# Optimization experiments

Hardware: AMD Instinct MI355X
Metric: run time of the kernel (lower is better)

## Reference

```python
import jax, jax.numpy as jnp
import numpy as np

NUM_NODES = 100000
OUT_CHANNELS = 64
NUM_EDGES = 3200000


def setup_inputs() -> dict:
    key = jax.random.key(0)
    k1, k2, k3 = jax.random.split(key, 3)
    edge_index = jax.random.randint(k1, (2, NUM_EDGES), 0, NUM_NODES, dtype=jnp.int64) if jax.config.jax_enable_x64 else jax.random.randint(k1, (2, NUM_EDGES), 0, NUM_NODES, dtype=jnp.int32)
    # nn.Linear default init: U(-1/sqrt(fan_in), 1/sqrt(fan_in)); use randn-scale for a correctness baseline
    W_weight = jax.random.normal(k2, (OUT_CHANNELS, NUM_NODES), dtype=jnp.float32) * (1.0 / np.sqrt(NUM_NODES))
    W_bias = jax.random.normal(k3, (OUT_CHANNELS,), dtype=jnp.float32) * (1.0 / np.sqrt(NUM_NODES))
    return {"edge_index": edge_index, "W_weight": W_weight, "W_bias": W_bias}


def reference(edge_index, W_weight, W_bias):
    # A is the [N, N] binary COO adjacency (duplicate edges sum, matching
    # an uncoalesced torch sparse COO matmul). logits = A @ W_weight.T + b.
    num_nodes = W_weight.shape[1]
    row = edge_index[0] - jnp.min(edge_index[0])  # row = row - row.min()
    col = edge_index[1]
    Wt = W_weight.T  # [N, C]
    # SpMM as gather + segment-sum: logits[i] = sum_{(i,j) in E} Wt[j]
    logits = jax.ops.segment_sum(Wt[col], row, num_segments=num_nodes)  # [N, C]
    logits = logits + W_bias
    return jax.nn.log_softmax(logits, axis=1)
```

## Files before the change

### kernel.cpp

```cpp
#include <hip/hip_runtime.h>
#include <hip/hip_bf16.h>
#include <hip/hip_fp8.h>
#include <limits.h>

#define NUM_NODES 100000
#define OUT_CH 64
#define NUM_EDGES 3200000
#define BROWS 64
#define BSHIFT 6
#define NBUCK 1563
#define NBUCK_EXT 3125
#define NPBLK 256
#define EPB (NUM_EDGES / NPBLK)
#define I4PB (EPB / 4)
#define STAGECAP 4096
#define NTRANS 1563
#define FP8_SCALE 256.0f
#define FP8_INV (1.0f / 256.0f)

typedef float v2f __attribute__((ext_vector_type(2)));

__device__ __forceinline__ float fp8_decode_slow(unsigned b) {
    unsigned s = b >> 7, e = (b >> 3) & 0xF, m = b & 7;
    float v = (e == 0) ? ldexpf((float)m, -9) : ldexpf((float)(8 + m), (int)e - 10);
    return s ? -v : v;
}

__global__ __launch_bounds__(256) void LINK_62689342652831_mth_kernel(
    const float* __restrict__ W, unsigned char* __restrict__ Wt8,
    const int* __restrict__ rows, int* __restrict__ minp, int* __restrict__ hist2d) {
    __shared__ float tile[64][65];
    if (blockIdx.x < NTRANS) {
        int n0 = blockIdx.x * 64;
        int tx = threadIdx.x & 63;
        int ty = threadIdx.x >> 6;
        for (int c = ty; c < 64; c += 4) {
            int n = n0 + tx;
            tile[c][tx] = (n < NUM_NODES) ? W[(size_t)c * NUM_NODES + n] : 0.0f;
        }
        __syncthreads();
        for (int i = ty; i < 64; i += 4) {
            int n = n0 + i;
            if (n < NUM_NODES) {
                __hip_fp8_e4m3 q(FP8_SCALE * tile[tx][i]);
                Wt8[(size_t)n * OUT_CH + tx] = *reinterpret_cast<unsigned char*>(&q);
            }
        }
    } else {
        int blk = blockIdx.x - NTRANS;
        int* h = (int*)tile;
        int* sm = (int*)tile + 2048;
        for (int i = threadIdx.x; i < NBUCK; i += 256) h[i] = 0;
        __syncthreads();
        const int4* r4 = (const int4*)rows;
        int m = INT_MAX;
        for (int i = threadIdx.x; i < I4PB; i += 256) {
            int4 v = r4[blk * I4PB + i];
            m = min(m, min(min(v.x, v.y), min(v.z, v.w)));
            atomicAdd(&h[(unsigned)v.x >> BSHIFT], 1);
            atomicAdd(&h[(unsigned)v.y >> BSHIFT], 1);
            atomicAdd(&h[(unsigned)v.z >> BSHIFT], 1);
            atomicAdd(&h[(unsigned)v.w >> BSHIFT], 1);
        }
        for (int off = 32; off > 0; off >>= 1) m = min(m, __shfl_xor(m, off, 64));
        if ((threadIdx.x & 63) == 0) sm[threadIdx.x >> 6] = m;
        __syncthreads();
        for (int i = threadIdx.x; i < NBUCK; i += 256) hist2d[blk * NBUCK + i] = h[i];
        if (threadIdx.x == 0)
            atomicMin(minp, min(min(sm[0], sm[1]), min(sm[2], sm[3])));
    }
}

__global__ __launch_bounds__(512) void LINK_62689342652831_colscan_kernel(
    int* __restrict__ hist2d, int* __restrict__ totals) {
    int lane = threadIdx.x & 63;
    int wid = threadIdx.x >> 6;
    int b = blockIdx.x * 8 + wid;
    if (b >= NBUCK) return;
    int carry = 0;
    for (int rnd = 0; rnd < NPBLK / 64; ++rnd) {
        int blk = rnd * 64 + lane;
        int v = hist2d[blk * NBUCK + b];
        int x = v;
        for (int off = 1; off < 64; off <<= 1) {
            int y = __shfl_up(x, off, 64);
            if (lane >= off) x += y;
        }
        hist2d[blk * NBUCK + b] = x - v + carry;
        carry += __shfl(x, 63, 64);
    }
    if (lane == 0) totals[b] = carry;
}

__global__ __launch_bounds__(1024) void LINK_62689342652831_bscan_kernel(
    const int* __restrict__ totals, int* __restrict__ bstart) {
    __shared__ int ss[1024];
    int t = threadIdx.x;
    int i0 = 2 * t, i1 = 2 * t + 1;
    int v0 = (i0 < NBUCK) ? totals[i0] : 0;
    int v1 = (i1 < NBUCK) ? totals[i1] : 0;
    int p1 = v0 + v1;
    ss[t] = p1;
    __syncthreads();
    for (int off = 1; off < 1024; off <<= 1) {
        int x = (t >= off) ? ss[t - off] : 0;
        __syncthreads();
        ss[t] += x;
        __syncthreads();
    }
    int texcl = ss[t] - p1;
    if (i0 < NBUCK) bstart[i0] = texcl;
    if (i1 < NBUCK) bstart[i1] = texcl + v0;
    if (t == 1023) bstart[NBUCK] = ss[1023];
}

__global__ __launch_bounds__(512) void LINK_62689342652831_part_kernel(
    const int* __restrict__ rows, const int* __restrict__ cols,
    const int* __restrict__ hist2d, const int* __restrict__ bstart,
    unsigned int* __restrict__ packed) {
    __shared__ int offs_l[NBUCK];
    __shared__ int lcur[NBUCK];
    int blk = blockIdx.x;
    for (int i = threadIdx.x; i < NBUCK; i += 512) {
        offs_l[i] = bstart[i] + hist2d[blk * NBUCK + i];
        lcur[i] = 0;
    }
    __syncthreads();
    const int4* r4 = (const int4*)rows;
    const int4* c4 = (const int4*)cols;
    for (int i = threadIdx.x; i < I4PB; i += 512) {
        int4 rv = r4[blk * I4PB + i];
        int4 cv = c4[blk * I4PB + i];
#pragma unroll
        for (int k = 0; k < 4; ++k) {
            int r = (k == 0) ? rv.x : (k == 1) ? rv.y : (k == 2) ? rv.z : rv.w;
            int c = (k == 0) ? cv.x : (k == 1) ? cv.y : (k == 2) ? cv.z : cv.w;
            int b = (unsigned)r >> BSHIFT;
            int pos = offs_l[b] + atomicAdd(&lcur[b], 1);
            packed[pos] = ((unsigned)(r & (BROWS - 1)) << 17) | (unsigned)c;
        }
    }
}

__global__ __launch_bounds__(256) void LINK_62689342652831_spmm_kernel(
    const unsigned int* __restrict__ packed, const int* __restrict__ bstart,
    const unsigned char* __restrict__ Wt8, const float* __restrict__ bias,
    const int* __restrict__ minp, float* __restrict__ out) {
    __shared__ unsigned int sorted[STAGECAP];
    __shared__ int rhist[BROWS];
    __shared__ int rstart[BROWS + 1];
    __shared__ int rcur[BROWS];

    int lane = threadIdx.x & 63;
    int wid = threadIdx.x >> 6;
    int b = blockIdx.x;
    int minv = *minp;
    if (b * BROWS - minv >= NUM_NODES) return;
    int s = 0, e = 0;
    if (b < NBUCK) { s = bstart[b]; e = bstart[b + 1]; }
    int n = e - s;

    if (n <= STAGECAP) {
        if (threadIdx.x < BROWS) rhist[threadIdx.x] = 0;
        __syncthreads();
        for (int i = threadIdx.x; i < n; i += 256)
            atomicAdd(&rhist[packed[s + i] >> 17], 1);
        __syncthreads();
        if (threadIdx.x < 64) {
            int c0 = rhist[lane];
            int x0 = c0;
            for (int off = 1; off < 64; off <<= 1) {
                int y0 = __shfl_up(x0, off, 64);
                if (lane >= off) x0 += y0;
            }
            rstart[lane] = x0 - c0;
            rcur[lane] = x0 - c0;
            if (lane == 63) rstart[64] = x0;
        }
        __syncthreads();
        for (int i = threadIdx.x; i < n; i += 256) {
            unsigned int u = packed[s + i];
            int pos = atomicAdd(&rcur[u >> 17], 1);
            sorted[pos] = u;
        }
        __syncthreads();

        const unsigned int* Wt1 = (const unsigned int*)Wt8;
        int q = lane >> 4;
        int ql = lane & 15;
        float b0 = bias[4 * ql], b1 = bias[4 * ql + 1],
              b2 = bias[4 * ql + 2], b3 = bias[4 * ql + 3];

        for (int r = wid; r < BROWS; r += 4) {
            int gr = b * BROWS + r - minv;
            if (gr < 0 || gr >= NUM_NODES) continue;
            int s0 = rstart[r], e0 = rstart[r + 1];
            float a0 = 0, a1 = 0, a2 = 0, a3 = 0;
            int i = s0 + q;
            for (; i + 4 < e0; i += 8) {
                unsigned int ua = sorted[i], ub = sorted[i + 4];
                unsigned int wa = Wt1[(size_t)(ua & 0x1FFFF) * 16 + ql];
                unsigned int wb = Wt1[(size_t)(ub & 0x1FFFF) * 16 + ql];
#if __has_builtin(__builtin_amdgcn_cvt_pk_f32_fp8)
                v2f la = __builtin_amdgcn_cvt_pk_f32_fp8((int)wa, false);
                v2f ha = __builtin_amdgcn_cvt_pk_f32_fp8((int)wa, true);
                v2f lb = __builtin_amdgcn_cvt_pk_f32_fp8((int)wb, false);
                v2f hb = __builtin_amdgcn_cvt_pk_f32_fp8((int)wb, true);
                a0 += la.x + lb.x; a1 += la.y + lb.y;
                a2 += ha.x + hb.x; a3 += ha.y + hb.y;
#else
                a0 += fp8_decode_slow(wa & 0xFF) + fp8_decode_slow(wb & 0xFF);
                a1 += fp8_decode_slow((wa >> 8) & 0xFF) + fp8_decode_slow((wb >> 8) & 0xFF);
                a2 += fp8_decode_slow((wa >> 16) & 0xFF) + fp8_decode_slow((wb >> 16) & 0xFF);
                a3 += fp8_decode_slow(wa >> 24) + fp8_decode_slow(wb >> 24);
#endif
            }
            for (; i < e0; i += 4) {
                unsigned int w = Wt1[(size_t)(sorted[i] & 0x1FFFF) * 16 + ql];
#if __has_builtin(__builtin_amdgcn_cvt_pk_f32_fp8)
                v2f lo = __builtin_amdgcn_cvt_pk_f32_fp8((int)w, false);
                v2f hi = __builtin_amdgcn_cvt_pk_f32_fp8((int)w, true);
                a0 += lo.x; a1 += lo.y; a2 += hi.x; a3 += hi.y;
#else
                a0 += fp8_decode_slow(w & 0xFF);
                a1 += fp8_decode_slow((w >> 8) & 0xFF);
                a2 += fp8_decode_slow((w >> 16) & 0xFF);
                a3 += fp8_decode_slow(w >> 24);
#endif
            }
            a0 += __shfl_xor(a0, 32, 64); a1 += __shfl_xor(a1, 32, 64);
            a2 += __shfl_xor(a2, 32, 64); a3 += __shfl_xor(a3, 32, 64);
            a0 += __shfl_xor(a0, 16, 64); a1 += __shfl_xor(a1, 16, 64);
            a2 += __shfl_xor(a2, 16, 64); a3 += __shfl_xor(a3, 16, 64);

            float x0 = a0 * FP8_INV + b0, x1 = a1 * FP8_INV + b1;
            float x2 = a2 * FP8_INV + b2, x3 = a3 * FP8_INV + b3;
            float m = fmaxf(fmaxf(x0, x1), fmaxf(x2, x3));
            for (int off = 8; off > 0; off >>= 1) m = fmaxf(m, __shfl_xor(m, off, 64));
            float ssum = expf(x0 - m) + expf(x1 - m) + expf(x2 - m) + expf(x3 - m);
            for (int off = 8; off > 0; off >>= 1) ssum += __shfl_xor(ssum, off, 64);
            float l = m + logf(ssum);
            if (lane < 16) {
                float4 o = {x0 - l, x1 - l, x2 - l, x3 - l};
                *(float4*)&out[(size_t)gr * OUT_CH + 4 * ql] = o;
            }
        }
    } else {
        float* acc = (float*)sorted;
        for (int i = threadIdx.x; i < BROWS * OUT_CH; i += 256) acc[i] = 0.0f;
        __syncthreads();
        for (int i = s + wid; i < e; i += 4) {
            unsigned int u = packed[i];
            float v = fp8_decode_slow(Wt8[(size_t)(u & 0x1FFFF) * OUT_CH + lane]);
            atomicAdd(&acc[(u >> 17) * OUT_CH + lane], v);
        }
        __syncthreads();
        float bsv = bias[lane];
        for (int r = wid; r < BROWS; r += 4) {
            int gr = b * BROWS + r - minv;
            if (gr < 0 || gr >= NUM_NODES) continue;
            float x = acc[r * OUT_CH + lane] * FP8_INV + bsv;
            float m = x;
            for (int off = 32; off > 0; off >>= 1) m = fmaxf(m, __shfl_xor(m, off, 64));
            float ex = expf(x - m);
            float ssum = ex;
            for (int off = 32; off > 0; off >>= 1) ssum += __shfl_xor(ssum, off, 64);
            out[(size_t)gr * OUT_CH + lane] = x - m - logf(ssum);
        }
    }
}

__global__ void LINK_62689342652831_minf_kernel(const int* __restrict__ rows, int n,
                                                int* __restrict__ minp) {
    int tid = blockIdx.x * blockDim.x + threadIdx.x;
    int stride = gridDim.x * blockDim.x;
    int m = INT_MAX;
    for (int i = tid; i < n; i += stride) m = min(m, rows[i]);
    for (int off = 32; off > 0; off >>= 1) m = min(m, __shfl_xor(m, off, 64));
    if ((threadIdx.x & 63) == 0) atomicMin(minp, m);
}

__global__ void LINK_62689342652831_scatter_kernel(const int* __restrict__ rows,
                                                   const int* __restrict__ cols,
                                                   const float* __restrict__ W,
                                                   const int* __restrict__ minp,
                                                   float* __restrict__ out) {
    int lane = threadIdx.x & 63;
    int gw = (blockIdx.x * blockDim.x + threadIdx.x) >> 6;
    int nw = (gridDim.x * blockDim.x) >> 6;
    int minv = *minp;
    for (int e = gw; e < NUM_EDGES; e += nw) {
        int r = rows[e] - minv;
        int c = cols[e];
        float v = W[(size_t)lane * NUM_NODES + c];
        unsafeAtomicAdd(&out[(size_t)r * 64 + lane], v);
    }
}

__global__ void LINK_62689342652831_logsoftmax_kernel(float* __restrict__ out,
                                                      const float* __restrict__ bias) {
    int lane = threadIdx.x & 63;
    int gw = (blockIdx.x * blockDim.x + threadIdx.x) >> 6;
    int nw = (gridDim.x * blockDim.x) >> 6;
    float b = bias[lane];
    for (int r = gw; r < NUM_NODES; r += nw) {
        float x = out[(size_t)r * 64 + lane] + b;
        float m = x;
        for (int off = 32; off > 0; off >>= 1) m = fmaxf(m, __shfl_xor(m, off, 64));
        float e = expf(x - m);
        float s = e;
        for (int off = 32; off > 0; off >>= 1) s += __shfl_xor(s, off, 64);
        out[(size_t)r * 64 + lane] = x - m - logf(s);
    }
}

extern "C" void kernel_launch(void* const* d_in, const int* in_sizes, int n_in,
                              void* d_out, int out_size, void* d_ws, size_t ws_size,
                              hipStream_t stream) {
    const int* edges = (const int*)d_in[0];
    const int* rows = edges;
    const int* cols = edges + NUM_EDGES;
    const float* W = (const float*)d_in[1];
    const float* bias = (const float*)d_in[2];
    float* out = (float*)d_out;

    char* ws = (char*)d_ws;
    const size_t OFF_MIN = 0;
    const size_t OFF_TOT = 1024;
    const size_t OFF_BSTART = 16384;
    const size_t OFF_H2D = 32768;
    const size_t OFF_PACKED = 2 * 1024 * 1024;
    const size_t OFF_WT8 = OFF_PACKED + (size_t)NUM_EDGES * 4;
    const size_t need = OFF_WT8 + (size_t)NUM_NODES * OUT_CH;

    int* minp = (int*)(ws + OFF_MIN);
    int* totals = (int*)(ws + OFF_TOT);
    int* bstart = (int*)(ws + OFF_BSTART);
    int* hist2d = (int*)(ws + OFF_H2D);
    unsigned int* packed = (unsigned int*)(ws + OFF_PACKED);
    unsigned char* Wt8 = (unsigned char*)(ws + OFF_WT8);

    hipMemsetAsync(minp, 0x7f, sizeof(int), stream);

    if (ws_size >= need) {
        LINK_62689342652831_mth_kernel<<<NTRANS + NPBLK, 256, 0, stream>>>(W, Wt8, rows,
                                                                           minp, hist2d);
        LINK_62689342652831_colscan_kernel<<<(NBUCK + 7) / 8, 512, 0, stream>>>(hist2d, totals);
        LINK_62689342652831_bscan_kernel<<<1, 1024, 0, stream>>>(totals, bstart);
        LINK_62689342652831_part_kernel<<<NPBLK, 512, 0, stream>>>(rows, cols, hist2d,
                                                                   bstart, packed);
        LINK_62689342652831_spmm_kernel<<<NBUCK_EXT, 256, 0, stream>>>(packed, bstart, Wt8,
                                                                       bias, minp, out);
    } else {
        LINK_62689342652831_minf_kernel<<<2048, 256, 0, stream>>>(rows, NUM_EDGES, minp);
        hipMemsetAsync(d_out, 0, (size_t)out_size * sizeof(float), stream);
        LINK_62689342652831_scatter_kernel<<<2048, 256, 0, stream>>>(rows, cols, W, minp, out);
        LINK_62689342652831_logsoftmax_kernel<<<4096, 256, 0, stream>>>(out, bias);
    }
}
```

Baseline: 127.4 us.

## Fuse transpose, histogram, scans and partition into one cooperative kernel

Replaces the four preprocessing kernels (transpose/histogram, column scan, bucket scan, partition) with a single cooperative launch that uses grid-wide syncs between phases. Each block keeps its packed (row,col) edge words in shared memory (EPB entries), so the partition phase does not reload the column array from global memory. This removes three kernel launches and their inter-kernel gaps. In exchange it relies on only 256 blocks, which must all be co-resident; this limits parallelism for the transpose and colscan phases and adds grid.sync costs. The large shared-memory footprint (about 50KB) lowers occupancy.

```diff
diff --git a/kernel.cpp b/kernel.cpp
--- a/kernel.cpp
+++ b/kernel.cpp
@@ -1,7 +1,10 @@
 #include <hip/hip_runtime.h>
 #include <hip/hip_bf16.h>
 #include <hip/hip_fp8.h>
+#include <hip/hip_cooperative_groups.h>
 #include <limits.h>
+
+namespace cg = cooperative_groups;
 
 #define NUM_NODES 100000
 #define OUT_CH 64
@@ -26,118 +29,138 @@
     return s ? -v : v;
 }
 
-__global__ __launch_bounds__(256) void LINK_62689342652831_mth_kernel(
+__global__ __launch_bounds__(512) void LINK_62689342652831_coop_kernel(
     const float* __restrict__ W, unsigned char* __restrict__ Wt8,
-    const int* __restrict__ rows, int* __restrict__ minp, int* __restrict__ hist2d) {
-    __shared__ float tile[64][65];
-    if (blockIdx.x < NTRANS) {
-        int n0 = blockIdx.x * 64;
-        int tx = threadIdx.x & 63;
-        int ty = threadIdx.x >> 6;
-        for (int c = ty; c < 64; c += 4) {
-            int n = n0 + tx;
-            tile[c][tx] = (n < NUM_NODES) ? W[(size_t)c * NUM_NODES + n] : 0.0f;
-        }
-        __syncthreads();
-        for (int i = ty; i < 64; i += 4) {
+    const int* __restrict__ rows, const int* __restrict__ cols,
+    int* __restrict__ minp, int* __restrict__ hist2d, int* __restrict__ totals,
+    int* __restrict__ bstart, unsigned int* __restrict__ packed) {
+    cg::grid_group grid = cg::this_grid();
+    __shared__ unsigned int pk[EPB];
+    __shared__ int h[NBUCK];
+    __shared__ int lcur[NBUCK];
+    __shared__ int sm8[8];
+
+    int tid = threadIdx.x;
+    int blk = blockIdx.x;
+    int lane = tid & 63;
+    int wid = tid >> 6;
+
+    float(*tile)[65] = (float(*)[65])pk;
+    for (int tb = blk; tb < NTRANS; tb += NPBLK) {
+        int n0 = tb * 64;
+        for (int c = wid; c < 64; c += 8) {
+            int n = n0 + lane;
+            tile[c][lane] = (n < NUM_NODES) ? W[(size_t)c * NUM_NODES + n] : 0.0f;
+        }
+        __syncthreads();
+        for (int i = wid; i < 64; i += 8) {
             int n = n0 + i;
             if (n < NUM_NODES) {
-                __hip_fp8_e4m3 q(FP8_SCALE * tile[tx][i]);
-                Wt8[(size_t)n * OUT_CH + tx] = *reinterpret_cast<unsigned char*>(&q);
-            }
-        }
-    } else {
-        int blk = blockIdx.x - NTRANS;
-        int* h = (int*)tile;
-        int* sm = (int*)tile + 2048;
-        for (int i = threadIdx.x; i < NBUCK; i += 256) h[i] = 0;
-        __syncthreads();
-        const int4* r4 = (const int4*)rows;
-        int m = INT_MAX;
-        for (int i = threadIdx.x; i < I4PB; i += 256) {
-            int4 v = r4[blk * I4PB + i];
-            m = min(m, min(min(v.x, v.y), min(v.z, v.w)));
-            atomicAdd(&h[(unsigned)v.x >> BSHIFT], 1);
-            atomicAdd(&h[(unsigned)v.y >> BSHIFT], 1);
-            atomicAdd(&h[(unsigned)v.z >> BSHIFT], 1);
-            atomicAdd(&h[(unsigned)v.w >> BSHIFT], 1);
-        }
-        for (int off = 32; off > 0; off >>= 1) m = min(m, __shfl_xor(m, off, 64));
-        if ((threadIdx.x & 63) == 0) sm[threadIdx.x >> 6] = m;
-        __syncthreads();
-        for (int i = threadIdx.x; i < NBUCK; i += 256) hist2d[blk * NBUCK + i] = h[i];
-        if (threadIdx.x == 0)
-            atomicMin(minp, min(min(sm[0], sm[1]), min(sm[2], sm[3])));
-    }
-}
-
-__global__ __launch_bounds__(512) void LINK_62689342652831_colscan_kernel(
-    int* __restrict__ hist2d, int* __restrict__ totals) {
-    int lane = threadIdx.x & 63;
-    int wid = threadIdx.x >> 6;
-    int b = blockIdx.x * 8 + wid;
-    if (b >= NBUCK) return;
-    int carry = 0;
-    for (int rnd = 0; rnd < NPBLK / 64; ++rnd) {
-        int blk = rnd * 64 + lane;
-        int v = hist2d[blk * NBUCK + b];
-        int x = v;
-        for (int off = 1; off < 64; off <<= 1) {
-            int y = __shfl_up(x, off, 64);
-            if (lane >= off) x += y;
-        }
-        hist2d[blk * NBUCK + b] = x - v + carry;
-        carry += __shfl(x, 63, 64);
-    }
-    if (lane == 0) totals[b] = carry;
-}
-
-__global__ __launch_bounds__(1024) void LINK_62689342652831_bscan_kernel(
-    const int* __restrict__ totals, int* __restrict__ bstart) {
-    __shared__ int ss[1024];
-    int t = threadIdx.x;
-    int i0 = 2 * t, i1 = 2 * t + 1;
-    int v0 = (i0 < NBUCK) ? totals[i0] : 0;
-    int v1 = (i1 < NBUCK) ? totals[i1] : 0;
-    int p1 = v0 + v1;
-    ss[t] = p1;
-    __syncthreads();
-    for (int off = 1; off < 1024; off <<= 1) {
-        int x = (t >= off) ? ss[t - off] : 0;
-        __syncthreads();
-        ss[t] += x;
-        __syncthreads();
-    }
-    int texcl = ss[t] - p1;
-    if (i0 < NBUCK) bstart[i0] = texcl;
-    if (i1 < NBUCK) bstart[i1] = texcl + v0;
-    if (t == 1023) bstart[NBUCK] = ss[1023];
-}
-
-__global__ __launch_bounds__(512) void LINK_62689342652831_part_kernel(
-    const int* __restrict__ rows, const int* __restrict__ cols,
-    const int* __restrict__ hist2d, const int* __restrict__ bstart,
-    unsigned int* __restrict__ packed) {
-    __shared__ int offs_l[NBUCK];
-    __shared__ int lcur[NBUCK];
-    int blk = blockIdx.x;
-    for (int i = threadIdx.x; i < NBUCK; i += 512) {
-        offs_l[i] = bstart[i] + hist2d[blk * NBUCK + i];
-        lcur[i] = 0;
-    }
+                __hip_fp8_e4m3 q(FP8_SCALE * tile[lane][i]);
+                Wt8[(size_t)n * OUT_CH + lane] = *reinterpret_cast<unsigned char*>(&q);
+            }
+        }
+        __syncthreads();
+    }
+
+    for (int i = tid; i < NBUCK; i += 512) h[i] = 0;
     __syncthreads();
     const int4* r4 = (const int4*)rows;
     const int4* c4 = (const int4*)cols;
-    for (int i = threadIdx.x; i < I4PB; i += 512) {
+    uint4* pk4 = (uint4*)pk;
+    int m = INT_MAX;
+    for (int i = tid; i < I4PB; i += 512) {
         int4 rv = r4[blk * I4PB + i];
         int4 cv = c4[blk * I4PB + i];
+        m = min(m, min(min(rv.x, rv.y), min(rv.z, rv.w)));
+        atomicAdd(&h[(unsigned)rv.x >> BSHIFT], 1);
+        atomicAdd(&h[(unsigned)rv.y >> BSHIFT], 1);
+        atomicAdd(&h[(unsigned)rv.z >> BSHIFT], 1);
+        atomicAdd(&h[(unsigned)rv.w >> BSHIFT], 1);
+        uint4 p;
+        p.x = ((unsigned)(rv.x & (BROWS - 1)) << 17) | (unsigned)cv.x;
+        p.y = ((unsigned)(rv.y & (BROWS - 1)) << 17) | (unsigned)cv.y;
+        p.z = ((unsigned)(rv.z & (BROWS - 1)) << 17) | (unsigned)cv.z;
+        p.w = ((unsigned)(rv.w & (BROWS - 1)) << 17) | (unsigned)cv.w;
+        pk4[i] = p;
+    }
+    for (int off = 32; off > 0; off >>= 1) m = min(m, __shfl_xor(m, off, 64));
+    if (lane == 0) sm8[wid] = m;
+    __syncthreads();
+    if (tid == 0) {
+        int mm = sm8[0];
+#pragma unroll
+        for (int k = 1; k < 8; ++k) mm = min(mm, sm8[k]);
+        atomicMin(minp, mm);
+    }
+    for (int i = tid; i < NBUCK; i += 512) hist2d[blk * NBUCK + i] = h[i];
+    grid.sync();
+
+    {
+        int b = blk * 8 + wid;
+        if (b < NBUCK) {
+            int carry = 0;
+            for (int rnd = 0; rnd < NPBLK / 64; ++rnd) {
+                int bb = rnd * 64 + lane;
+                int v = hist2d[bb * NBUCK + b];
+                int x = v;
+                for (int off = 1; off < 64; off <<= 1) {
+                    int y = __shfl_up(x, off, 64);
+                    if (lane >= off) x += y;
+                }
+                hist2d[bb * NBUCK + b] = x - v + carry;
+                carry += __shfl(x, 63, 64);
+            }
+            if (lane == 0) totals[b] = carry;
+        }
+    }
+    grid.sync();
+
+    if (blk == 0) {
+        int* ss = lcur;
+        int v0 = 0, v1 = 0, v2 = 0, v3 = 0;
+        int base = tid * 4;
+        if (base + 0 < NBUCK) v0 = totals[base + 0];
+        if (base + 1 < NBUCK) v1 = totals[base + 1];
+        if (base + 2 < NBUCK) v2 = totals[base + 2];
+        if (base + 3 < NBUCK) v3 = totals[base + 3];
+        int run = v0 + v1 + v2 + v3;
+        ss[tid] = run;
+        __syncthreads();
+        for (int off = 1; off < 512; off <<= 1) {
+            int x = (tid >= off) ? ss[tid - off] : 0;
+            __syncthreads();
+            ss[tid] += x;
+            __syncthreads();
+        }
+        int acc = ss[tid] - run;
+        if (base + 0 < NBUCK) bstart[base + 0] = acc;
+        acc += v0;
+        if (base + 1 < NBUCK) bstart[base + 1] = acc;
+        acc += v1;
+        if (base + 2 < NBUCK) bstart[base + 2] = acc;
+        acc += v2;
+        if (base + 3 < NBUCK) bstart[base + 3] = acc;
+        acc += v3;
+        if (tid == 511) bstart[NBUCK] = acc;
+    }
+    grid.sync();
+
+    for (int i = tid; i < NBUCK; i += 512) {
+        h[i] = bstart[i] + hist2d[blk * NBUCK + i];
+        lcur[i] = 0;
+    }
+    __syncthreads();
+    for (int i = tid; i < I4PB; i += 512) {
+        int4 rv = r4[blk * I4PB + i];
+        uint4 p = pk4[i];
 #pragma unroll
         for (int k = 0; k < 4; ++k) {
             int r = (k == 0) ? rv.x : (k == 1) ? rv.y : (k == 2) ? rv.z : rv.w;
-            int c = (k == 0) ? cv.x : (k == 1) ? cv.y : (k == 2) ? cv.z : cv.w;
+            unsigned pv = (k == 0) ? p.x : (k == 1) ? p.y : (k == 2) ? p.z : p.w;
             int b = (unsigned)r >> BSHIFT;
-            int pos = offs_l[b] + atomicAdd(&lcur[b], 1);
-            packed[pos] = ((unsigned)(r & (BROWS - 1)) << 17) | (unsigned)c;
+            int pos = h[b] + atomicAdd(&lcur[b], 1);
+            packed[pos] = pv;
         }
     }
 }
@@ -343,12 +366,11 @@
     hipMemsetAsync(minp, 0x7f, sizeof(int), stream);
 
     if (ws_size >= need) {
-        LINK_62689342652831_mth_kernel<<<NTRANS + NPBLK, 256, 0, stream>>>(W, Wt8, rows,
-                                                                           minp, hist2d);
-        LINK_62689342652831_colscan_kernel<<<(NBUCK + 7) / 8, 512, 0, stream>>>(hist2d, totals);
-        LINK_62689342652831_bscan_kernel<<<1, 1024, 0, stream>>>(totals, bstart);
-        LINK_62689342652831_part_kernel<<<NPBLK, 512, 0, stream>>>(rows, cols, hist2d,
-                                                                   bstart, packed);
+        void* args[] = {(void*)&W, (void*)&Wt8, (void*)&rows, (void*)&cols,
+                        (void*)&minp, (void*)&hist2d, (void*)&totals,
+                        (void*)&bstart, (void*)&packed};
+        hipLaunchCooperativeKernel((const void*)LINK_62689342652831_coop_kernel,
+                                   dim3(NPBLK), dim3(512), args, 0, stream);
         LINK_62689342652831_spmm_kernel<<<NBUCK_EXT, 256, 0, stream>>>(packed, bstart, Wt8,
                                                                        bias, minp, out);
     } else {
```

Result: slower. 236.4 us (+85.5%).
